# Kernel optimization log

Hardware: AMD Instinct MI355X
Metric: run time of the kernel (lower is better)

## Reference

```python
import jax, jax.numpy as jnp
import numpy as np

DIM = 256
N = 8192

def setup_inputs() -> dict:
    key = jax.random.key(0)
    kx, kq, kk, kv = jax.random.split(key, 4)
    X = jax.random.normal(kx, (N, DIM), dtype=jnp.float32)
    # nn.Linear weights are [out, in]; xavier-uniform-like scale via normal/sqrt(dim)
    Wq = jax.random.normal(kq, (DIM, DIM), dtype=jnp.float32) / np.sqrt(DIM)
    Wk = jax.random.normal(kk, (DIM, DIM), dtype=jnp.float32) / np.sqrt(DIM)
    Wv = jax.random.normal(kv, (DIM, DIM), dtype=jnp.float32) / np.sqrt(DIM)
    return {"X": X, "Wq": Wq, "Wk": Wk, "Wv": Wv}

def reference(X, Wq, Wk, Wv):
    # nn.Linear(no bias): y = X @ W.T
    Q = X @ Wq.T  # [N, D]
    K = X @ Wk.T
    V = X @ Wv.T
    scores = (Q @ K.T) / jnp.sqrt(jnp.asarray(DIM, dtype=X.dtype))  # [N, N]
    softed = jax.nn.softmax(scores, axis=-1)
    return softed @ V  # [N, D]
```

## Files before the change

kernel.cpp:

```cpp
#include <hip/hip_runtime.h>
#include <math.h>

#define N 8192
#define D 256
#define QBLK 256
#define KBLK 64

typedef float f32x4 __attribute__((ext_vector_type(4)));
typedef short bf16x8 __attribute__((ext_vector_type(8)));

#define MFMA(a, b, c) __builtin_amdgcn_mfma_f32_16x16x32_bf16((a), (b), (c), 0, 0, 0)

__device__ __forceinline__ unsigned short f2b(float f) {
    unsigned u = __builtin_bit_cast(unsigned, f);
    u = u + 0x7fffu + ((u >> 16) & 1u);
    return (unsigned short)(u >> 16);
}
__device__ __forceinline__ unsigned pk2(float a, float b) {
    return (unsigned)f2b(a) | ((unsigned)f2b(b) << 16);
}
__device__ __forceinline__ unsigned cvtpk(float a, float b) {
    unsigned r;
    asm("v_cvt_pk_bf16_f32 %0, %1, %2" : "=v"(r) : "v"(a), "v"(b));
    return r;
}
__device__ __forceinline__ float b2f(short s) {
    unsigned x = ((unsigned)(unsigned short)s) << 16;
    return __builtin_bit_cast(float, x);
}

__global__ __launch_bounds__(256) void proj_mfma(
    const float* __restrict__ X, const float* __restrict__ Wq,
    const float* __restrict__ Wk, const float* __restrict__ Wv,
    unsigned short* __restrict__ Qb, unsigned short* __restrict__ Kb,
    unsigned short* __restrict__ Vt)
{
    __shared__ char Wl[32768];
    const int z = blockIdx.z;
    const float* W = (z == 0) ? Wq : (z == 1) ? Wk : Wv;
    const int r0 = blockIdx.x * 64;
    const int c0 = blockIdx.y * 64;
    const int t = threadIdx.x, w = t >> 6, l = t & 63;
    const int lo = l & 15, hi = l >> 4;

    #pragma unroll
    for (int i = 0; i < 16; ++i) {
        int e4 = t + i * 256;
        int col = e4 >> 6, kk4 = e4 & 63;
        float4 f = *(const float4*)&W[(size_t)(c0 + col) * D + kk4 * 4];
        unsigned long long v = (unsigned long long)pk2(f.x, f.y)
                             | ((unsigned long long)pk2(f.z, f.w) << 32);
        *(unsigned long long*)(Wl + col * 512 + ((kk4 * 8) ^ ((col & 7) << 4))) = v;
    }
    __syncthreads();

    bf16x8 xf[8];
    {
        const float* xr = X + (size_t)(r0 + w * 16 + lo) * D;
        #pragma unroll
        for (int ks = 0; ks < 8; ++ks) {
            float4 a = *(const float4*)(xr + ks * 32 + hi * 8);
            float4 b = *(const float4*)(xr + ks * 32 + hi * 8 + 4);
            bf16x8 v;
            v[0] = (short)f2b(a.x); v[1] = (short)f2b(a.y);
            v[2] = (short)f2b(a.z); v[3] = (short)f2b(a.w);
            v[4] = (short)f2b(b.x); v[5] = (short)f2b(b.y);
            v[6] = (short)f2b(b.z); v[7] = (short)f2b(b.w);
            xf[ks] = v;
        }
    }

    f32x4 acc[4];
    #pragma unroll
    for (int nc = 0; nc < 4; ++nc) acc[nc] = (f32x4){0.f, 0.f, 0.f, 0.f};
    #pragma unroll
    for (int ks = 0; ks < 8; ++ks) {
        #pragma unroll
        for (int nc = 0; nc < 4; ++nc) {
            int col = nc * 16 + lo;
            bf16x8 wf = *(const bf16x8*)(Wl + col * 512 +
                                         ((ks * 64 + hi * 16) ^ ((col & 7) << 4)));
            acc[nc] = MFMA(xf[ks], wf, acc[nc]);
        }
    }

    if (z < 2) {
        unsigned short* Y = z ? Kb : Qb;
        #pragma unroll
        for (int nc = 0; nc < 4; ++nc)
            #pragma unroll
            for (int r = 0; r < 4; ++r)
                Y[(size_t)(r0 + w * 16 + hi * 4 + r) * D + c0 + nc * 16 + lo] = f2b(acc[nc][r]);
    } else {
        #pragma unroll
        for (int nc = 0; nc < 4; ++nc) {
            unsigned long long v = (unsigned long long)pk2(acc[nc][0], acc[nc][1])
                                 | ((unsigned long long)pk2(acc[nc][2], acc[nc][3]) << 32);
            *(unsigned long long*)&Vt[(size_t)(c0 + nc * 16 + lo) * N + r0 + w * 16 + hi * 4] = v;
        }
    }
}

__device__ __forceinline__ void stage_tile8(
    const unsigned short* __restrict__ Kb, const unsigned short* __restrict__ Vt,
    char* kbuf, char* vbuf, int kt, int t)
{
    #pragma unroll
    for (int i = 0; i < 4; ++i) {
        int c = t + i * 512;
        {
            int row = c >> 5, xc = c & 31;
            int pk = ((row >> 5) << 5) | (((row >> 2) & 3) << 3)
                   | (((row >> 4) & 1) << 2) | (row & 3);
            const unsigned short* gp = Kb + (size_t)(kt + pk) * D + (xc ^ (row & 7)) * 8;
            __builtin_amdgcn_global_load_lds(
                (const __attribute__((address_space(1))) void*)gp,
                (__attribute__((address_space(3))) void*)(kbuf + c * 16), 16, 0, 0);
        }
        {
            int dd = c >> 3, xc = c & 7;
            const unsigned short* gp = Vt + (size_t)dd * N + kt + (xc ^ (dd & 7)) * 8;
            __builtin_amdgcn_global_load_lds(
                (const __attribute__((address_space(1))) void*)gp,
                (__attribute__((address_space(3))) void*)(vbuf + c * 16), 16, 0, 0);
        }
    }
}

template <int KSPLIT>
__global__ __launch_bounds__(512, 2) void attn_mfma(
    const unsigned short* __restrict__ Qb,
    const unsigned short* __restrict__ Kb,
    const unsigned short* __restrict__ Vt,
    unsigned short* __restrict__ Opart,
    float2* __restrict__ ml)
{
    extern __shared__ char smem[];
    const int t = threadIdx.x;
    const int w = t >> 6;
    const int l = t & 63;
    const int lo = l & 15;
    const int hi = l >> 4;
    const int q0 = blockIdx.x * QBLK + w * 32;
    const int split = blockIdx.y;
    const int kbase = split * (N / KSPLIT);
    const int NTS = N / KSPLIT / KBLK;

    bf16x8 qf[2][8];
    #pragma unroll
    for (int s = 0; s < 2; ++s) {
        const unsigned short* qrow = Qb + (size_t)(q0 + s * 16 + lo) * D;
        #pragma unroll
        for (int ks = 0; ks < 8; ++ks)
            qf[s][ks] = *(const bf16x8*)(qrow + ks * 32 + hi * 8);
    }

    stage_tile8(Kb, Vt, smem, smem + 65536, kbase, t);

    f32x4 Oacc[2][16];
    #pragma unroll
    for (int s = 0; s < 2; ++s)
        #pragma unroll
        for (int i = 0; i < 16; ++i) Oacc[s][i] = (f32x4){0.f, 0.f, 0.f, 0.f};
    float m_run[2] = {-INFINITY, -INFINITY};
    float l_run[2] = {0.f, 0.f};
    const float scale = 0.0625f;

    __syncthreads();

    for (int tt = 0; tt < NTS; ++tt) {
        const int cur = tt & 1;
        if (tt + 1 < NTS)
            stage_tile8(Kb, Vt, smem + (cur ^ 1) * 32768,
                        smem + 65536 + (cur ^ 1) * 32768,
                        kbase + (tt + 1) * KBLK, t);

        const char* Kl = smem + cur * 32768;
        const char* Vl = smem + 65536 + cur * 32768;

        f32x4 sacc[2][4];
        #pragma unroll
        for (int s = 0; s < 2; ++s)
            #pragma unroll
            for (int kg = 0; kg < 4; ++kg) sacc[s][kg] = (f32x4){0.f, 0.f, 0.f, 0.f};
        __builtin_amdgcn_s_setprio(1);
        #pragma unroll
        for (int ks = 0; ks < 8; ++ks) {
            #pragma unroll
            for (int kg = 0; kg < 4; ++kg) {
                int key = kg * 16 + lo;
                bf16x8 kf = *(const bf16x8*)(Kl + key * 512 +
                                             ((ks * 64 + hi * 16) ^ ((key & 7) << 4)));
                sacc[0][kg] = MFMA(kf, qf[0][ks], sacc[0][kg]);
                sacc[1][kg] = MFMA(kf, qf[1][ks], sacc[1][kg]);
            }
        }
        __builtin_amdgcn_s_setprio(0);

        float mx[2];
        #pragma unroll
        for (int s = 0; s < 2; ++s) {
            float m = -INFINITY;
            #pragma unroll
            for (int kg = 0; kg < 4; ++kg)
                #pragma unroll
                for (int r = 0; r < 4; ++r) m = fmaxf(m, sacc[s][kg][r]);
            m *= scale;
            m = fmaxf(m, __shfl_xor(m, 16));
            m = fmaxf(m, __shfl_xor(m, 32));
            mx[s] = m;
        }

        bool need = (mx[0] > m_run[0] + 8.0f) || (mx[1] > m_run[1] + 8.0f);
        if (__any(need)) {
            #pragma unroll
            for (int s = 0; s < 2; ++s) {
                float m_new = fmaxf(m_run[s], mx[s]);
                float corr = __expf(m_run[s] - m_new);
                m_run[s] = m_new;
                l_run[s] *= corr;
                float cr0 = __shfl(corr, hi * 4 + 0);
                float cr1 = __shfl(corr, hi * 4 + 1);
                float cr2 = __shfl(corr, hi * 4 + 2);
                float cr3 = __shfl(corr, hi * 4 + 3);
                #pragma unroll
                for (int nc = 0; nc < 16; ++nc) {
                    Oacc[s][nc][0] *= cr0; Oacc[s][nc][1] *= cr1;
                    Oacc[s][nc][2] *= cr2; Oacc[s][nc][3] *= cr3;
                }
            }
        }

        bf16x8 pa[2][2];
        #pragma unroll
        for (int s = 0; s < 2; ++s) {
            float p[16];
            float ts = 0.f;
            #pragma unroll
            for (int kg = 0; kg < 4; ++kg)
                #pragma unroll
                for (int r = 0; r < 4; ++r) {
                    float pv = __expf(sacc[s][kg][r] * scale - m_run[s]);
                    p[kg * 4 + r] = pv;
                    ts += pv;
                }
            ts += __shfl_xor(ts, 16);
            ts += __shfl_xor(ts, 32);
            l_run[s] += ts;

            union { unsigned u[4]; bf16x8 v; } u0, u1;
            #pragma unroll
            for (int j = 0; j < 4; ++j) {
                u0.u[j] = cvtpk(p[j * 2], p[j * 2 + 1]);
                u1.u[j] = cvtpk(p[8 + j * 2], p[8 + j * 2 + 1]);
            }
            pa[s][0] = u0.v;
            pa[s][1] = u1.v;
        }

        __builtin_amdgcn_s_setprio(1);
        #pragma unroll
        for (int nc = 0; nc < 16; ++nc) {
            int dd = nc * 16 + lo;
            bf16x8 v0 = *(const bf16x8*)(Vl + dd * 128 + ((hi * 16) ^ ((dd & 7) << 4)));
            bf16x8 v1 = *(const bf16x8*)(Vl + dd * 128 + ((64 + hi * 16) ^ ((dd & 7) << 4)));
            Oacc[0][nc] = MFMA(pa[0][0], v0, Oacc[0][nc]);
            Oacc[0][nc] = MFMA(pa[0][1], v1, Oacc[0][nc]);
            Oacc[1][nc] = MFMA(pa[1][0], v0, Oacc[1][nc]);
            Oacc[1][nc] = MFMA(pa[1][1], v1, Oacc[1][nc]);
        }
        __builtin_amdgcn_s_setprio(0);

        __syncthreads();
    }

    #pragma unroll
    for (int s = 0; s < 2; ++s) {
        const int qrow = q0 + s * 16 + hi * 4;
        #pragma unroll
        for (int nc = 0; nc < 16; ++nc)
            #pragma unroll
            for (int r = 0; r < 4; ++r)
                Opart[((size_t)split * N + qrow + r) * D + nc * 16 + lo] = f2b(Oacc[s][nc][r]);
        if (hi == 0)
            ml[(size_t)split * N + q0 + s * 16 + lo] = make_float2(m_run[s], l_run[s]);
    }
}

__global__ __launch_bounds__(256) void combine_kernel(
    const unsigned short* __restrict__ Opart, const float2* __restrict__ ml,
    float* __restrict__ out, int nsplit)
{
    int idx = blockIdx.x * 256 + threadIdx.x;
    int q = idx >> 5;
    int d0 = (idx & 31) * 8;

    float M = -INFINITY;
    for (int i = 0; i < nsplit; ++i) M = fmaxf(M, ml[(size_t)i * N + q].x);
    float L = 0.f;
    float acc[8] = {};
    for (int i = 0; i < nsplit; ++i) {
        float2 v = ml[(size_t)i * N + q];
        float wgt = __expf(v.x - M);
        L += wgt * v.y;
        bf16x8 ov = *(const bf16x8*)&Opart[((size_t)i * N + q) * D + d0];
        #pragma unroll
        for (int j = 0; j < 8; ++j) acc[j] += wgt * b2f(ov[j]);
    }
    float r = 1.f / L;
    #pragma unroll
    for (int j = 0; j < 8; ++j) out[(size_t)q * D + d0 + j] = acc[j] * r;
}

extern "C" void kernel_launch(void* const* d_in, const int* in_sizes, int n_in,
                              void* d_out, int out_size, void* d_ws, size_t ws_size,
                              hipStream_t stream) {
    const float* X  = (const float*)d_in[0];
    const float* Wq = (const float*)d_in[1];
    const float* Wk = (const float*)d_in[2];
    const float* Wv = (const float*)d_in[3];

    unsigned short* ws = (unsigned short*)d_ws;
    const size_t ndq = (size_t)N * D;
    unsigned short* Qb = ws;
    unsigned short* Kb = ws + ndq;
    unsigned short* Vt = ws + 2 * ndq;
    unsigned short* Opart = ws + 3 * ndq;

    auto need = [ndq](int ks) {
        return (size_t)(3 + ks) * ndq * 2 + (size_t)ks * N * 8;
    };
    const int ksplit = (ws_size >= need(8)) ? 8 : (ws_size >= need(4)) ? 4 : 2;
    float2* ml = (float2*)(ws + (3 + ksplit) * ndq);

    (void)hipFuncSetAttribute((const void*)attn_mfma<8>,
                              hipFuncAttributeMaxDynamicSharedMemorySize, 131072);
    (void)hipFuncSetAttribute((const void*)attn_mfma<4>,
                              hipFuncAttributeMaxDynamicSharedMemorySize, 131072);
    (void)hipFuncSetAttribute((const void*)attn_mfma<2>,
                              hipFuncAttributeMaxDynamicSharedMemorySize, 131072);

    proj_mfma<<<dim3(N / 64, D / 64, 3), 256, 0, stream>>>(X, Wq, Wk, Wv, Qb, Kb, Vt);
    if (ksplit == 8)
        attn_mfma<8><<<dim3(N / QBLK, 8), 512, 131072, stream>>>(Qb, Kb, Vt, Opart, ml);
    else if (ksplit == 4)
        attn_mfma<4><<<dim3(N / QBLK, 4), 512, 131072, stream>>>(Qb, Kb, Vt, Opart, ml);
    else
        attn_mfma<2><<<dim3(N / QBLK, 2), 512, 131072, stream>>>(Qb, Kb, Vt, Opart, ml);
    combine_kernel<<<(N * D / 8) / 256, 256, 0, stream>>>(Opart, ml, (float*)d_out, ksplit);
}
```

Baseline: 128.7 us.

## Prefetch two tiles ahead with manual waitcnt barriers and exp2-domain softmax

```diff
diff --git a/kernel.cpp b/kernel.cpp
--- a/kernel.cpp
+++ b/kernel.cpp
@@ -10,6 +10,7 @@
 typedef short bf16x8 __attribute__((ext_vector_type(8)));
 
 #define MFMA(a, b, c) __builtin_amdgcn_mfma_f32_16x16x32_bf16((a), (b), (c), 0, 0, 0)
+#define BAR() __builtin_amdgcn_s_barrier()
 
 __device__ __forceinline__ unsigned short f2b(float f) {
     unsigned u = __builtin_bit_cast(unsigned, f);
@@ -156,6 +157,7 @@
     }
 
     stage_tile8(Kb, Vt, smem, smem + 65536, kbase, t);
+    stage_tile8(Kb, Vt, smem + 32768, smem + 65536 + 32768, kbase + KBLK, t);
 
     f32x4 Oacc[2][16];
     #pragma unroll
@@ -164,17 +166,13 @@
         for (int i = 0; i < 16; ++i) Oacc[s][i] = (f32x4){0.f, 0.f, 0.f, 0.f};
     float m_run[2] = {-INFINITY, -INFINITY};
     float l_run[2] = {0.f, 0.f};
-    const float scale = 0.0625f;
-
-    __syncthreads();
+    const float scale2 = 0.09016994f;
+
+    asm volatile("s_waitcnt vmcnt(8)" ::: "memory");
+    BAR();
 
     for (int tt = 0; tt < NTS; ++tt) {
         const int cur = tt & 1;
-        if (tt + 1 < NTS)
-            stage_tile8(Kb, Vt, smem + (cur ^ 1) * 32768,
-                        smem + 65536 + (cur ^ 1) * 32768,
-                        kbase + (tt + 1) * KBLK, t);
-
         const char* Kl = smem + cur * 32768;
         const char* Vl = smem + 65536 + cur * 32768;
 
@@ -205,18 +203,18 @@
             for (int kg = 0; kg < 4; ++kg)
                 #pragma unroll
                 for (int r = 0; r < 4; ++r) m = fmaxf(m, sacc[s][kg][r]);
-            m *= scale;
-            m = fmaxf(m, __shfl_xor(m, 16));
-            m = fmaxf(m, __shfl_xor(m, 32));
-            mx[s] = m;
-        }
-
-        bool need = (mx[0] > m_run[0] + 8.0f) || (mx[1] > m_run[1] + 8.0f);
-        if (__any(need)) {
+            mx[s] = m * scale2;
+        }
+
+        bool need = (mx[0] > m_run[0] + 11.0f) || (mx[1] > m_run[1] + 11.0f);
+        if (__builtin_expect(__any(need), 0)) {
             #pragma unroll
             for (int s = 0; s < 2; ++s) {
-                float m_new = fmaxf(m_run[s], mx[s]);
-                float corr = __expf(m_run[s] - m_new);
+                float m = mx[s];
+                m = fmaxf(m, __shfl_xor(m, 16));
+                m = fmaxf(m, __shfl_xor(m, 32));
+                float m_new = fmaxf(m_run[s], m);
+                float corr = exp2f(m_run[s] - m_new);
                 m_run[s] = m_new;
                 l_run[s] *= corr;
                 float cr0 = __shfl(corr, hi * 4 + 0);
@@ -232,22 +230,20 @@
         }
 
         bf16x8 pa[2][2];
+        float ts[2];
         #pragma unroll
         for (int s = 0; s < 2; ++s) {
             float p[16];
-            float ts = 0.f;
+            float sum = 0.f;
             #pragma unroll
             for (int kg = 0; kg < 4; ++kg)
                 #pragma unroll
                 for (int r = 0; r < 4; ++r) {
-                    float pv = __expf(sacc[s][kg][r] * scale - m_run[s]);
+                    float pv = exp2f(sacc[s][kg][r] * scale2 - m_run[s]);
                     p[kg * 4 + r] = pv;
-                    ts += pv;
+                    sum += pv;
                 }
-            ts += __shfl_xor(ts, 16);
-            ts += __shfl_xor(ts, 32);
-            l_run[s] += ts;
-
+            ts[s] = sum;
             union { unsigned u[4]; bf16x8 v; } u0, u1;
             #pragma unroll
             for (int j = 0; j < 4; ++j) {
@@ -271,9 +267,27 @@
         }
         __builtin_amdgcn_s_setprio(0);
 
-        __syncthreads();
-    }
-
+        l_run[0] += ts[0];
+        l_run[1] += ts[1];
+
+        asm volatile("" ::: "memory");
+        BAR();
+        if (tt + 2 < NTS) {
+            stage_tile8(Kb, Vt, smem + cur * 32768, smem + 65536 + cur * 32768,
+                        kbase + (tt + 2) * KBLK, t);
+            asm volatile("s_waitcnt vmcnt(8)" ::: "memory");
+            BAR();
+        } else if (tt + 1 < NTS) {
+            asm volatile("s_waitcnt vmcnt(0)" ::: "memory");
+            BAR();
+        }
+    }
+
+    #pragma unroll
+    for (int s = 0; s < 2; ++s) {
+        l_run[s] += __shfl_xor(l_run[s], 16);
+        l_run[s] += __shfl_xor(l_run[s], 32);
+    }
     #pragma unroll
     for (int s = 0; s < 2; ++s) {
         const int qrow = q0 + s * 16 + hi * 4;
@@ -301,7 +315,7 @@
     float acc[8] = {};
     for (int i = 0; i < nsplit; ++i) {
         float2 v = ml[(size_t)i * N + q];
-        float wgt = __expf(v.x - M);
+        float wgt = exp2f(v.x - M);
         L += wgt * v.y;
         bf16x8 ov = *(const bf16x8*)&Opart[((size_t)i * N + q) * D + d0];
         #pragma unroll
```

Measured after the change: 134.4 us. +4.4%, slower.
